# Kernel tuning notes

Hardware: AMD Instinct MI355X
Metric: run time of the kernel (lower is better)

The kernel has to match this reference:

```python
import jax, jax.numpy as jnp
import numpy as np

TEMP = 0.2
NUM_PATCH, BATCH, DIM = 16, 512, 2048


def _l2_normalize(x, axis=-1, eps=1e-12):
    # matches torch F.normalize: x / max(||x||, eps)
    norm = jnp.linalg.norm(x, axis=axis, keepdims=True)
    return x / jnp.maximum(norm, eps)


def setup_inputs() -> dict:
    key = jax.random.key(0)
    features = jax.random.normal(key, (NUM_PATCH, BATCH, DIM), dtype=jnp.float32)
    return {"features": features}


def reference(features) -> jnp.ndarray:
    P, B, D = features.shape
    # z_avg: mean over the num_patch crops -> [B, D]
    z_avg = _l2_normalize(features.mean(axis=0), axis=1)
    # concat crops along batch -> [P*B, D], then L2 normalize rows
    f = _l2_normalize(features.reshape(P * B, D), axis=1)
    # similarity matrix [P*B, B]
    sim = f @ z_avg.T
    # labels = identity(B) tiled P times along rows => positive of row i is column i % B.
    # CE with target 0 after concat([pos, negs]) == -pos/T + logsumexp(all/T)
    rows = jnp.arange(P * B)
    pos = sim[rows, rows % B]
    logits = sim / TEMP
    loss = jnp.mean(jax.nn.logsumexp(logits, axis=1) - pos / TEMP)
    return loss
```

## Files before the change

### kernel.cpp

```cpp
#include <hip/hip_runtime.h>
#include <hip/hip_bf16.h>
#include <math.h>

#define NP 16
#define NB 512
#define ND 2048
#define NM (NP*NB)
#define BM 128
#define BN 128
#define BK 64
#define NS (ND/BK)
#define NCB (NB/BN)

typedef __attribute__((ext_vector_type(4))) float f32x4;
typedef unsigned int u32;

__device__ inline float dot4(float4 v) {
    return v.x * v.x + v.y * v.y + v.z * v.z + v.w * v.w;
}

#if __has_builtin(__builtin_amdgcn_cvt_pk_fp8_f32)
__device__ inline u32 pack4_fp8(float a, float b, float c, float d) {
    int w = 0;
    w = __builtin_amdgcn_cvt_pk_fp8_f32(a, b, w, false);
    w = __builtin_amdgcn_cvt_pk_fp8_f32(c, d, w, true);
    return (u32)w;
}
#else
#include <hip/hip_fp8.h>
__device__ inline u32 pack4_fp8(float a, float b, float c, float d) {
    u32 w  = (u32)__hip_cvt_float_to_fp8(a, __HIP_SATFINITE, __HIP_E4M3);
    w |= (u32)__hip_cvt_float_to_fp8(b, __HIP_SATFINITE, __HIP_E4M3) << 8;
    w |= (u32)__hip_cvt_float_to_fp8(c, __HIP_SATFINITE, __HIP_E4M3) << 16;
    w |= (u32)__hip_cvt_float_to_fp8(d, __HIP_SATFINITE, __HIP_E4M3) << 24;
    return w;
}
#endif

__global__ __launch_bounds__(512) void prep_kernel(
        const float* __restrict__ feat,
        unsigned char* __restrict__ an,
        unsigned char* __restrict__ zn) {
    const int b = blockIdx.x, tid = threadIdx.x;
    const int lane = tid & 63, wv = tid >> 6;
    const float4* feat4 = (const float4*)feat;

    float4 zp[8];
#pragma unroll
    for (int it = 0; it < 8; ++it) zp[it] = make_float4(0.f, 0.f, 0.f, 0.f);

#pragma unroll
    for (int j = 0; j < 2; ++j) {
        const int p = wv * 2 + j;
        const size_t row = (size_t)p * NB + b;
        const float4* rp = feat4 + row * (ND / 4);
        float4 rv[8];
        float ss = 0.f;
#pragma unroll
        for (int it = 0; it < 8; ++it) {
            rv[it] = rp[it * 64 + lane];
            ss += dot4(rv[it]);
            zp[it].x += rv[it].x; zp[it].y += rv[it].y;
            zp[it].z += rv[it].z; zp[it].w += rv[it].w;
        }
#pragma unroll
        for (int off = 32; off > 0; off >>= 1) ss += __shfl_xor(ss, off);
        const float inv = 1.f / fmaxf(sqrtf(ss), 1e-12f);
        u32* wp = (u32*)(an + row * ND);
#pragma unroll
        for (int it = 0; it < 8; ++it)
            wp[it * 64 + lane] = pack4_fp8(rv[it].x * inv, rv[it].y * inv,
                                           rv[it].z * inv, rv[it].w * inv);
    }

    __shared__ float4 zl[8][512];
#pragma unroll
    for (int it = 0; it < 8; ++it) zl[wv][it * 64 + lane] = zp[it];
    __syncthreads();

    float4 z = zl[0][tid];
#pragma unroll
    for (int v = 1; v < 8; ++v) {
        float4 t = zl[v][tid];
        z.x += t.x; z.y += t.y; z.z += t.z; z.w += t.w;
    }
    float ss = dot4(z);
#pragma unroll
    for (int off = 32; off > 0; off >>= 1) ss += __shfl_xor(ss, off);
    __shared__ float wpart[8];
    __shared__ float invz_s;
    if (lane == 0) wpart[wv] = ss;
    __syncthreads();
    if (tid == 0) {
        float t = 0.f;
#pragma unroll
        for (int v = 0; v < 8; ++v) t += wpart[v];
        invz_s = 1.f / fmaxf(sqrtf(t), 1e-12f);
    }
    __syncthreads();
    const float iz = invz_s;
    ((u32*)(zn + (size_t)b * ND))[tid] =
        pack4_fp8(z.x * iz, z.y * iz, z.z * iz, z.w * iz);
}

__global__ __launch_bounds__(512, 1) void gemm_loss_kernel(
        const unsigned char* __restrict__ an,
        const unsigned char* __restrict__ zn,
        float* __restrict__ pmax_g,
        float* __restrict__ psum_g,
        float* __restrict__ ppos_g) {
    __shared__ __align__(16) unsigned char abuf[3 * BM * BK];
    __shared__ __align__(16) unsigned char bbuf[3 * BN * BK];
    __shared__ float sm_max[BM][4];
    __shared__ float sm_sum[BM][4];
    __shared__ float sm_pos[BM];

    const int tid  = threadIdx.x;
    const int lane = tid & 63;
    const int w    = tid >> 6;
    const int wr   = w >> 2;
    const int wc   = w & 3;
    const int l15  = lane & 15;
    const int l4   = lane >> 4;
    const int cb   = blockIdx.x & (NCB - 1);
    const int brow = (blockIdx.x >> 2) * BM;
    const int bcol = cb * BN;

    f32x4 acc[4][2] = {};

    const int sr  = tid >> 2;
    const int scs = (tid & 3) ^ ((sr >> 2) & 3);
    const unsigned char* asrc = an + (size_t)(brow + sr) * ND + scs * 16;
    const unsigned char* bsrc = zn + (size_t)(bcol + sr) * ND + scs * 16;

#define STAGE(BI, S) do {                                                     \
        const int koB_ = (S) * BK;                                            \
        __builtin_amdgcn_global_load_lds((const u32*)(asrc + koB_),           \
            (u32*)(&abuf[(BI) * 8192 + tid * 16]), 16, 0, 0);                 \
        __builtin_amdgcn_global_load_lds((const u32*)(bsrc + koB_),           \
            (u32*)(&bbuf[(BI) * 8192 + tid * 16]), 16, 0, 0);                 \
    } while (0)

    STAGE(0, 0);
    STAGE(1, 1);

    int acur = 0, astg = 2;
    for (int s = 0; s < NS; ++s) {
        if (s + 1 < NS) asm volatile("s_waitcnt vmcnt(2)" ::: "memory");
        else            asm volatile("s_waitcnt vmcnt(0)" ::: "memory");
        __builtin_amdgcn_sched_barrier(0);
        __builtin_amdgcn_s_barrier();
        __builtin_amdgcn_sched_barrier(0);

        long long af[2][4], bf[2][2];
#pragma unroll
        for (int kc = 0; kc < 2; ++kc) {
            const int kk = kc * 4 + l4;
#pragma unroll
            for (int m = 0; m < 4; ++m) {
                int r = wr * 64 + m * 16 + l15;
                int g = (kk >> 1) ^ ((r >> 2) & 3);
                af[kc][m] = *(const long long*)(
                    &abuf[acur * 8192 + r * 64 + g * 16 + (kk & 1) * 8]);
            }
#pragma unroll
            for (int n = 0; n < 2; ++n) {
                int r = wc * 32 + n * 16 + l15;
                int g = (kk >> 1) ^ ((r >> 2) & 3);
                bf[kc][n] = *(const long long*)(
                    &bbuf[acur * 8192 + r * 64 + g * 16 + (kk & 1) * 8]);
            }
        }

        if (s + 2 < NS) STAGE(astg, s + 2);

        __builtin_amdgcn_s_setprio(1);
#pragma unroll
        for (int kc = 0; kc < 2; ++kc)
#pragma unroll
        for (int m = 0; m < 4; ++m)
#pragma unroll
        for (int n = 0; n < 2; ++n)
            acc[m][n] = __builtin_amdgcn_mfma_f32_16x16x32_fp8_fp8(
                af[kc][m], bf[kc][n], acc[m][n], 0, 0, 0);
        __builtin_amdgcn_s_setprio(0);

        acur = (acur == 2) ? 0 : acur + 1;
        astg = (astg == 2) ? 0 : astg + 1;
    }
#undef STAGE

#pragma unroll
    for (int m = 0; m < 4; ++m) {
#pragma unroll
        for (int r = 0; r < 4; ++r) {
            const int lrow = wr * 64 + m * 16 + l4 * 4 + r;
            float lg[2];
            float mx = -1e30f;
#pragma unroll
            for (int n = 0; n < 2; ++n) {
                lg[n] = acc[m][n][r] * 5.0f;
                mx = fmaxf(mx, lg[n]);
            }
            mx = fmaxf(mx, __shfl_xor(mx, 1));
            mx = fmaxf(mx, __shfl_xor(mx, 2));
            mx = fmaxf(mx, __shfl_xor(mx, 4));
            mx = fmaxf(mx, __shfl_xor(mx, 8));
            float se = 0.f;
#pragma unroll
            for (int n = 0; n < 2; ++n) se += __expf(lg[n] - mx);
            se += __shfl_xor(se, 1);
            se += __shfl_xor(se, 2);
            se += __shfl_xor(se, 4);
            se += __shfl_xor(se, 8);
            if (l15 == 0) { sm_max[lrow][wc] = mx; sm_sum[lrow][wc] = se; }
            const int posc = (brow + lrow) & (NB - 1);
#pragma unroll
            for (int n = 0; n < 2; ++n)
                if (bcol + wc * 32 + n * 16 + l15 == posc) sm_pos[lrow] = lg[n];
        }
    }
    __syncthreads();

    if (tid < BM) {
        const int lrow = tid;
        const int grow = brow + lrow;
        float gm = -1e30f;
#pragma unroll
        for (int c = 0; c < 4; ++c) gm = fmaxf(gm, sm_max[lrow][c]);
        float tot = 0.f;
#pragma unroll
        for (int c = 0; c < 4; ++c)
            tot += sm_sum[lrow][c] * __expf(sm_max[lrow][c] - gm);
        pmax_g[cb * NM + grow] = gm;
        psum_g[cb * NM + grow] = tot;
        if (((grow & (NB - 1)) >> 7) == cb) ppos_g[grow] = sm_pos[lrow];
    }
}

__global__ __launch_bounds__(256) void reduce_kernel(
        const float* __restrict__ pmax_g, const float* __restrict__ psum_g,
        const float* __restrict__ ppos_g, float* __restrict__ part) {
    const int row = blockIdx.x * 256 + threadIdx.x;
    float mxs[NCB];
    float gm = -1e30f;
#pragma unroll
    for (int c = 0; c < NCB; ++c) {
        mxs[c] = pmax_g[c * NM + row];
        gm = fmaxf(gm, mxs[c]);
    }
    float tot = 0.f;
#pragma unroll
    for (int c = 0; c < NCB; ++c)
        tot += psum_g[c * NM + row] * __expf(mxs[c] - gm);
    float term = gm + __logf(tot) - ppos_g[row];
#pragma unroll
    for (int off = 32; off > 0; off >>= 1) term += __shfl_xor(term, off);
    __shared__ float wsum[4];
    const int lane = threadIdx.x & 63, wv = threadIdx.x >> 6;
    if (lane == 0) wsum[wv] = term;
    __syncthreads();
    if (threadIdx.x == 0)
        part[blockIdx.x] = wsum[0] + wsum[1] + wsum[2] + wsum[3];
}

__global__ void finalize_kernel(const float* __restrict__ part,
                                float* __restrict__ out) {
    const int lane = threadIdx.x;
    float v = (lane < 32) ? part[lane] : 0.f;
#pragma unroll
    for (int off = 32; off > 0; off >>= 1) v += __shfl_xor(v, off);
    if (lane == 0) out[0] = v * (1.0f / (float)NM);
}

extern "C" void kernel_launch(void* const* d_in, const int* in_sizes, int n_in,
                              void* d_out, int out_size, void* d_ws, size_t ws_size,
                              hipStream_t stream) {
    const float* feat = (const float*)d_in[0];

    unsigned char* an = (unsigned char*)d_ws;
    unsigned char* zn = an + (size_t)NM * ND;
    float* pmax = (float*)(zn + (size_t)NB * ND);
    float* psum = pmax + NCB * NM;
    float* ppos = psum + NCB * NM;
    float* part = ppos + NM;

    prep_kernel<<<NB, 512, 0, stream>>>(feat, an, zn);
    gemm_loss_kernel<<<(NM / BM) * NCB, 512, 0, stream>>>(an, zn, pmax, psum, ppos);
    reduce_kernel<<<NM / 256, 256, 0, stream>>>(pmax, psum, ppos, part);
    finalize_kernel<<<1, 64, 0, stream>>>(part, (float*)d_out);
}
```

Measured before the change: 47.83 us.

## Shrink GEMM row tile to 64 with 256-thread blocks and fuse finalize via atomics

```diff
diff --git a/kernel.cpp b/kernel.cpp
--- a/kernel.cpp
+++ b/kernel.cpp
@@ -6,7 +6,7 @@
 #define NB 512
 #define ND 2048
 #define NM (NP*NB)
-#define BM 128
+#define BM 64
 #define BN 128
 #define BK 64
 #define NS (ND/BK)
@@ -103,7 +103,7 @@
         pack4_fp8(z.x * iz, z.y * iz, z.z * iz, z.w * iz);
 }
 
-__global__ __launch_bounds__(512, 1) void gemm_loss_kernel(
+__global__ __launch_bounds__(256, 2) void gemm_loss_kernel(
         const unsigned char* __restrict__ an,
         const unsigned char* __restrict__ zn,
         float* __restrict__ pmax_g,
@@ -111,34 +111,44 @@
         float* __restrict__ ppos_g) {
     __shared__ __align__(16) unsigned char abuf[3 * BM * BK];
     __shared__ __align__(16) unsigned char bbuf[3 * BN * BK];
-    __shared__ float sm_max[BM][4];
-    __shared__ float sm_sum[BM][4];
+    __shared__ float sm_max[BM][2];
+    __shared__ float sm_sum[BM][2];
     __shared__ float sm_pos[BM];
 
     const int tid  = threadIdx.x;
     const int lane = tid & 63;
     const int w    = tid >> 6;
-    const int wr   = w >> 2;
-    const int wc   = w & 3;
+    const int wr   = w >> 1;
+    const int wc   = w & 1;
     const int l15  = lane & 15;
     const int l4   = lane >> 4;
     const int cb   = blockIdx.x & (NCB - 1);
     const int brow = (blockIdx.x >> 2) * BM;
     const int bcol = cb * BN;
 
-    f32x4 acc[4][2] = {};
-
-    const int sr  = tid >> 2;
-    const int scs = (tid & 3) ^ ((sr >> 2) & 3);
-    const unsigned char* asrc = an + (size_t)(brow + sr) * ND + scs * 16;
-    const unsigned char* bsrc = zn + (size_t)(bcol + sr) * ND + scs * 16;
+    f32x4 acc[2][4] = {};
+
+    const int sra = tid >> 2;
+    const int sca = (tid & 3) ^ ((sra >> 2) & 3);
+    const unsigned char* asrc = an + (size_t)(brow + sra) * ND + sca * 16;
+    const unsigned char* bsrc0;
+    const unsigned char* bsrc1;
+    {
+        int q0 = tid, q1 = 256 + tid;
+        int r0 = q0 >> 2, c0 = (q0 & 3) ^ ((r0 >> 2) & 3);
+        int r1 = q1 >> 2, c1 = (q1 & 3) ^ ((r1 >> 2) & 3);
+        bsrc0 = zn + (size_t)(bcol + r0) * ND + c0 * 16;
+        bsrc1 = zn + (size_t)(bcol + r1) * ND + c1 * 16;
+    }
 
 #define STAGE(BI, S) do {                                                     \
         const int koB_ = (S) * BK;                                            \
         __builtin_amdgcn_global_load_lds((const u32*)(asrc + koB_),           \
-            (u32*)(&abuf[(BI) * 8192 + tid * 16]), 16, 0, 0);                 \
-        __builtin_amdgcn_global_load_lds((const u32*)(bsrc + koB_),           \
+            (u32*)(&abuf[(BI) * 4096 + tid * 16]), 16, 0, 0);                 \
+        __builtin_amdgcn_global_load_lds((const u32*)(bsrc0 + koB_),          \
             (u32*)(&bbuf[(BI) * 8192 + tid * 16]), 16, 0, 0);                 \
+        __builtin_amdgcn_global_load_lds((const u32*)(bsrc1 + koB_),          \
+            (u32*)(&bbuf[(BI) * 8192 + 4096 + tid * 16]), 16, 0, 0);          \
     } while (0)
 
     STAGE(0, 0);
@@ -146,26 +156,26 @@
 
     int acur = 0, astg = 2;
     for (int s = 0; s < NS; ++s) {
-        if (s + 1 < NS) asm volatile("s_waitcnt vmcnt(2)" ::: "memory");
+        if (s + 1 < NS) asm volatile("s_waitcnt vmcnt(3)" ::: "memory");
         else            asm volatile("s_waitcnt vmcnt(0)" ::: "memory");
         __builtin_amdgcn_sched_barrier(0);
         __builtin_amdgcn_s_barrier();
         __builtin_amdgcn_sched_barrier(0);
 
-        long long af[2][4], bf[2][2];
+        long long af[2][2], bf[2][4];
 #pragma unroll
         for (int kc = 0; kc < 2; ++kc) {
             const int kk = kc * 4 + l4;
 #pragma unroll
-            for (int m = 0; m < 4; ++m) {
-                int r = wr * 64 + m * 16 + l15;
+            for (int m = 0; m < 2; ++m) {
+                int r = wr * 32 + m * 16 + l15;
                 int g = (kk >> 1) ^ ((r >> 2) & 3);
                 af[kc][m] = *(const long long*)(
-                    &abuf[acur * 8192 + r * 64 + g * 16 + (kk & 1) * 8]);
+                    &abuf[acur * 4096 + r * 64 + g * 16 + (kk & 1) * 8]);
             }
 #pragma unroll
-            for (int n = 0; n < 2; ++n) {
-                int r = wc * 32 + n * 16 + l15;
+            for (int n = 0; n < 4; ++n) {
+                int r = wc * 64 + n * 16 + l15;
                 int g = (kk >> 1) ^ ((r >> 2) & 3);
                 bf[kc][n] = *(const long long*)(
                     &bbuf[acur * 8192 + r * 64 + g * 16 + (kk & 1) * 8]);
@@ -178,9 +188,9 @@
 #pragma unroll
         for (int kc = 0; kc < 2; ++kc)
 #pragma unroll
-        for (int m = 0; m < 4; ++m)
-#pragma unroll
-        for (int n = 0; n < 2; ++n)
+        for (int m = 0; m < 2; ++m)
+#pragma unroll
+        for (int n = 0; n < 4; ++n)
             acc[m][n] = __builtin_amdgcn_mfma_f32_16x16x32_fp8_fp8(
                 af[kc][m], bf[kc][n], acc[m][n], 0, 0, 0);
         __builtin_amdgcn_s_setprio(0);
@@ -191,14 +201,14 @@
 #undef STAGE
 
 #pragma unroll
-    for (int m = 0; m < 4; ++m) {
+    for (int m = 0; m < 2; ++m) {
 #pragma unroll
         for (int r = 0; r < 4; ++r) {
-            const int lrow = wr * 64 + m * 16 + l4 * 4 + r;
-            float lg[2];
+            const int lrow = wr * 32 + m * 16 + l4 * 4 + r;
+            float lg[4];
             float mx = -1e30f;
 #pragma unroll
-            for (int n = 0; n < 2; ++n) {
+            for (int n = 0; n < 4; ++n) {
                 lg[n] = acc[m][n][r] * 5.0f;
                 mx = fmaxf(mx, lg[n]);
             }
@@ -208,7 +218,7 @@
             mx = fmaxf(mx, __shfl_xor(mx, 8));
             float se = 0.f;
 #pragma unroll
-            for (int n = 0; n < 2; ++n) se += __expf(lg[n] - mx);
+            for (int n = 0; n < 4; ++n) se += __expf(lg[n] - mx);
             se += __shfl_xor(se, 1);
             se += __shfl_xor(se, 2);
             se += __shfl_xor(se, 4);
@@ -216,8 +226,8 @@
             if (l15 == 0) { sm_max[lrow][wc] = mx; sm_sum[lrow][wc] = se; }
             const int posc = (brow + lrow) & (NB - 1);
 #pragma unroll
-            for (int n = 0; n < 2; ++n)
-                if (bcol + wc * 32 + n * 16 + l15 == posc) sm_pos[lrow] = lg[n];
+            for (int n = 0; n < 4; ++n)
+                if (bcol + wc * 64 + n * 16 + l15 == posc) sm_pos[lrow] = lg[n];
         }
     }
     __syncthreads();
@@ -225,13 +235,10 @@
     if (tid < BM) {
         const int lrow = tid;
         const int grow = brow + lrow;
-        float gm = -1e30f;
-#pragma unroll
-        for (int c = 0; c < 4; ++c) gm = fmaxf(gm, sm_max[lrow][c]);
-        float tot = 0.f;
-#pragma unroll
-        for (int c = 0; c < 4; ++c)
-            tot += sm_sum[lrow][c] * __expf(sm_max[lrow][c] - gm);
+        const float m0 = sm_max[lrow][0], m1 = sm_max[lrow][1];
+        const float gm = fmaxf(m0, m1);
+        const float tot = sm_sum[lrow][0] * __expf(m0 - gm)
+                        + sm_sum[lrow][1] * __expf(m1 - gm);
         pmax_g[cb * NM + grow] = gm;
         psum_g[cb * NM + grow] = tot;
         if (((grow & (NB - 1)) >> 7) == cb) ppos_g[grow] = sm_pos[lrow];
@@ -240,7 +247,8 @@
 
 __global__ __launch_bounds__(256) void reduce_kernel(
         const float* __restrict__ pmax_g, const float* __restrict__ psum_g,
-        const float* __restrict__ ppos_g, float* __restrict__ part) {
+        const float* __restrict__ ppos_g, float* __restrict__ acc_g,
+        u32* __restrict__ counter, float* __restrict__ out) {
     const int row = blockIdx.x * 256 + threadIdx.x;
     float mxs[NCB];
     float gm = -1e30f;
@@ -260,17 +268,15 @@
     const int lane = threadIdx.x & 63, wv = threadIdx.x >> 6;
     if (lane == 0) wsum[wv] = term;
     __syncthreads();
-    if (threadIdx.x == 0)
-        part[blockIdx.x] = wsum[0] + wsum[1] + wsum[2] + wsum[3];
-}
-
-__global__ void finalize_kernel(const float* __restrict__ part,
-                                float* __restrict__ out) {
-    const int lane = threadIdx.x;
-    float v = (lane < 32) ? part[lane] : 0.f;
-#pragma unroll
-    for (int off = 32; off > 0; off >>= 1) v += __shfl_xor(v, off);
-    if (lane == 0) out[0] = v * (1.0f / (float)NM);
+    if (threadIdx.x == 0) {
+        atomicAdd(acc_g, wsum[0] + wsum[1] + wsum[2] + wsum[3]);
+        __threadfence();
+        u32 old = atomicAdd(counter, 1u);
+        if (old == 31u) {
+            float total = atomicAdd(acc_g, 0.0f);
+            out[0] = total * (1.0f / (float)NM);
+        }
+    }
 }
 
 extern "C" void kernel_launch(void* const* d_in, const int* in_sizes, int n_in,
@@ -283,10 +289,13 @@
     float* pmax = (float*)(zn + (size_t)NB * ND);
     float* psum = pmax + NCB * NM;
     float* ppos = psum + NCB * NM;
-    float* part = ppos + NM;
+    float* accg = ppos + NM;
+    u32*   cntr = (u32*)(accg + 1);
+
+    hipMemsetAsync(accg, 0, 8, stream);
 
     prep_kernel<<<NB, 512, 0, stream>>>(feat, an, zn);
-    gemm_loss_kernel<<<(NM / BM) * NCB, 512, 0, stream>>>(an, zn, pmax, psum, ppos);
-    reduce_kernel<<<NM / 256, 256, 0, stream>>>(pmax, psum, ppos, part);
-    finalize_kernel<<<1, 64, 0, stream>>>(part, (float*)d_out);
-}
+    gemm_loss_kernel<<<(NM / BM) * NCB, 256, 0, stream>>>(an, zn, pmax, psum, ppos);
+    reduce_kernel<<<NM / 256, 256, 0, stream>>>(pmax, psum, ppos, accg, cntr,
+                                                (float*)d_out);
+}
```

After: 48.14 us. Within noise of the previous version (+0.6%).
